# Performance work log

Measured on AMD Instinct MI355X. Metric: run time of the kernel, lower is better.

Reference implementation:

```python
import jax, jax.numpy as jnp
import numpy as np

B, S, H, V, T, L = 32, 128, 1024, 32000, 50, 3


def _ln(x, g, b, eps=1e-5):
    m = x.mean(-1, keepdims=True)
    v = ((x - m) ** 2).mean(-1, keepdims=True)
    return (x - m) / jnp.sqrt(v + eps) * g + b


def setup_inputs() -> dict:
    key = jax.random.key(0)
    ks = iter(jax.random.split(key, 48))
    r = lambda shape, s=0.02: jax.random.normal(next(ks), shape, jnp.float32) * s
    return dict(
        encoder_outputs=jax.random.normal(next(ks), (B, S, H), jnp.float32),
        h0=jax.random.normal(next(ks), (L, B, H), jnp.float32),
        c0=jax.random.normal(next(ks), (L, B, H), jnp.float32),
        valid_src_len=jax.random.randint(next(ks), (B,), 1, S + 1),
        target=jax.random.randint(next(ks), (B, T), 0, V),
        embedding=r((V, H), 1.0),
        Wa=r((H, H)), ba=jnp.zeros((H,)),
        Ua=r((H, H)), ub=jnp.zeros((H,)),
        Va=r((1, H)), vb=jnp.zeros((1,)),
        temperature=jnp.ones((1,)),
        Wih0=r((4 * H, 2 * H)), Whh0=r((4 * H, H)), bih0=jnp.zeros((4 * H,)), bhh0=jnp.zeros((4 * H,)),
        Wih1=r((4 * H, H)), Whh1=r((4 * H, H)), bih1=jnp.zeros((4 * H,)), bhh1=jnp.zeros((4 * H,)),
        Wih2=r((4 * H, H)), Whh2=r((4 * H, H)), bih2=jnp.zeros((4 * H,)), bhh2=jnp.zeros((4 * H,)),
        fc_w=r((V, H)), fc_b=jnp.zeros((V,)),
        eng=jnp.ones((H,)), enb=jnp.zeros((H,)),
        cng=jnp.ones((H,)), cnb=jnp.zeros((H,)),
        ong=jnp.ones((H,)), onb=jnp.zeros((H,)),
    )


def _decode(encoder_outputs, h0, c0, valid_src_len, target, p):
    mask = jnp.arange(S)[None, :] < valid_src_len[:, None]           # (B,S)
    Ukeys = encoder_outputs @ p['Ua'].T + p['ub']                    # (B,S,H) precomputed Ua(keys)
    Wih = (p['Wih0'], p['Wih1'], p['Wih2'])
    Whh = (p['Whh0'], p['Whh1'], p['Whh2'])
    bih = (p['bih0'], p['bih1'], p['bih2'])
    bhh = (p['bhh0'], p['bhh1'], p['bhh2'])
    # teacher forcing: token at step t is start_token (0) for t=0, else target[:, t-1]
    tokens = jnp.concatenate([jnp.zeros((B, 1), target.dtype), target[:, :-1]], 1).T  # (T,B)

    def step(carry, tok):
        h, c = carry                                                 # each (L,B,H)
        emb = _ln(p['embedding'][tok], p['eng'], p['enb'])           # (B,H); dropout omitted (eval)
        q = h[-1]                                                    # (B,H) query = top-layer h
        s = jnp.tanh((q @ p['Wa'].T + p['ba'])[:, None, :] + Ukeys)  # (B,S,H)
        scores = (jnp.einsum('bsh,h->bs', s, p['Va'][0]) + p['vb'][0]) / p['temperature'][0]
        scores = jnp.where(mask, scores, -1e9)
        w = jax.nn.softmax(scores, axis=-1)                          # (B,S)
        ctx = _ln(jnp.einsum('bs,bsh->bh', w, encoder_outputs), p['cng'], p['cnb'])
        x = jnp.concatenate([emb, ctx], axis=-1)                     # (B,2H)
        hs, cs = [], []
        for l in range(L):                                           # 3 stacked LSTM layers
            g = x @ Wih[l].T + bih[l] + h[l] @ Whh[l].T + bhh[l]
            i_, f_, g_, o_ = jnp.split(g, 4, axis=-1)                # torch gate order i,f,g,o
            cl = jax.nn.sigmoid(f_) * c[l] + jax.nn.sigmoid(i_) * jnp.tanh(g_)
            hl = jax.nn.sigmoid(o_) * jnp.tanh(cl)
            hs.append(hl); cs.append(cl); x = hl
        out = _ln(x, p['ong'], p['onb'])
        logits = out @ p['fc_w'].T + p['fc_b']                       # (B,V)
        return (jnp.stack(hs), jnp.stack(cs)), (logits, w)

    (hT, cT), (logits, attn) = jax.lax.scan(step, (h0, c0), tokens)
    return logits.transpose(1, 0, 2), hT, cT, attn.transpose(1, 0, 2)


def reference(encoder_outputs, h0, c0, valid_src_len, target, embedding, Wa, ba, Ua, ub, Va, vb,
              temperature, Wih0, Whh0, bih0, bhh0, Wih1, Whh1, bih1, bhh1, Wih2, Whh2, bih2, bhh2,
              fc_w, fc_b, eng, enb, cng, cnb, ong, onb):
    p = dict(embedding=embedding, Wa=Wa, ba=ba, Ua=Ua, ub=ub, Va=Va, vb=vb, temperature=temperature,
             Wih0=Wih0, Whh0=Whh0, bih0=bih0, bhh0=bhh0, Wih1=Wih1, Whh1=Whh1, bih1=bih1, bhh1=bhh1,
             Wih2=Wih2, Whh2=Whh2, bih2=bih2, bhh2=bhh2, fc_w=fc_w, fc_b=fc_b,
             eng=eng, enb=enb, cng=cng, cnb=cnb, ong=ong, onb=onb)
    logits, hT, cT, attn = _decode(encoder_outputs, h0, c0, valid_src_len, target, p)
    return logits, (hT, cT), attn
```

## Files before the change

kernel.cpp:

```cpp
#include <hip/hip_runtime.h>
#include <math.h>

#define DEV_INLINE __device__ __forceinline__

constexpr int B = 32, S = 128, H = 1024, V = 32000, T = 50, L = 3;
constexpr int H2 = 2 * H, H4 = 4 * H;
constexpr int BH = B * H;

constexpr size_t HT_OFF   = (size_t)B * T * V;
constexpr size_t CT_OFF   = HT_OFF + (size_t)L * B * H;
constexpr size_t ATTN_OFF = CT_OFF + (size_t)L * B * H;

constexpr size_t WS_UKBF  = 0;
constexpr size_t WS_ENCBF = WS_UKBF + (size_t)B * S * H / 2;
constexpr size_t WS_EMBBF = WS_ENCBF + (size_t)B * S * H / 2;
constexpr size_t WS_H2ALL = WS_EMBBF + (size_t)T * BH / 2;
constexpr size_t WS_H     = WS_H2ALL + (size_t)T * BH;
constexpr size_t WS_C     = WS_H + (size_t)L * BH;
constexpr size_t WS_QWA   = WS_C + (size_t)L * BH;
constexpr size_t WS_SCO   = WS_QWA + (size_t)BH;
constexpr size_t WS_GAT   = WS_SCO + (size_t)B * S;
constexpr size_t WS_HBF   = WS_GAT + (size_t)B * H4;
constexpr size_t WS_XCBF  = WS_HBF + (size_t)2 * L * BH / 2;
constexpr size_t WS_OLALL = WS_XCBF + (size_t)B * H2 / 2;
constexpr size_t WS_WBF   = WS_OLALL + (size_t)T * BH / 2;

constexpr size_t OW_WA   = 0;
constexpr size_t OW_WIH0 = OW_WA   + (size_t)H * H;
constexpr size_t OW_WHH0 = OW_WIH0 + (size_t)H4 * H2;
constexpr size_t OW_WIH1 = OW_WHH0 + (size_t)H4 * H;
constexpr size_t OW_WHH1 = OW_WIH1 + (size_t)H4 * H;
constexpr size_t OW_WIH2 = OW_WHH1 + (size_t)H4 * H;
constexpr size_t OW_WHH2 = OW_WIH2 + (size_t)H4 * H;
constexpr size_t OW_FCW  = OW_WHH2 + (size_t)H4 * H;
constexpr size_t OW_UA   = OW_FCW  + (size_t)V * H;
constexpr size_t OW_END  = OW_UA   + (size_t)H * H;
constexpr size_t NEED_WS_BYTES = WS_WBF * 4 + OW_END * 2;

typedef __attribute__((ext_vector_type(8))) short short8;
typedef __attribute__((ext_vector_type(4))) float f32x4;
typedef __attribute__((ext_vector_type(4))) unsigned short u16x4;
typedef __attribute__((ext_vector_type(8))) unsigned short u16x8;

DEV_INLINE float sigmoidf_(float x) { return 1.f / (1.f + expf(-x)); }

DEV_INLINE unsigned short bf16u(float f) {
  union { float f; unsigned u; } v; v.f = f;
  unsigned r = v.u + 0x7fffu + ((v.u >> 16) & 1u);
  return (unsigned short)(r >> 16);
}
DEV_INLINE float bf2f(unsigned short u) {
  union { unsigned u; float f; } v; v.u = (unsigned)u << 16;
  return v.f;
}

DEV_INLINE float wave_sum(float v) {
#pragma unroll
  for (int o = 32; o; o >>= 1) v += __shfl_xor(v, o, 64);
  return v;
}

DEV_INLINE float blk_sum256(float v, float* buf) {
  v = wave_sum(v);
  __syncthreads();
  if ((threadIdx.x & 63) == 0) buf[threadIdx.x >> 6] = v;
  __syncthreads();
  return buf[0] + buf[1] + buf[2] + buf[3];
}

__global__ void k_init(const float* __restrict__ h0, const float* __restrict__ c0,
                       float* __restrict__ hst, float* __restrict__ cst,
                       unsigned short* __restrict__ hbf) {
  int idx = blockIdx.x * 256 + threadIdx.x;
  if (idx < L * BH) { hst[idx] = h0[idx]; hbf[idx] = bf16u(h0[idx]); }
  else cst[idx - L * BH] = c0[idx - L * BH];
}

__global__ void k_fin(const float* __restrict__ hst, const float* __restrict__ h2src,
                      const float* __restrict__ cst, float* __restrict__ out) {
  int idx = blockIdx.x * 256 + threadIdx.x;
  if (idx < 2 * BH) out[HT_OFF + idx] = hst[idx];
  else if (idx < 3 * BH) out[HT_OFF + idx] = h2src[idx - 2 * BH];
  else out[HT_OFF + idx] = cst[idx - 3 * BH];
}

constexpr int NCVT = 10;
struct CvtArgs { const float* src[NCVT]; unsigned short* dst[NCVT]; };
constexpr int CV_N4[NCVT] = {
  H * H / 4, H4 * H2 / 4, H4 * H / 4, H4 * H / 4, H4 * H / 4,
  H4 * H / 4, H4 * H / 4, V * H / 4, H * H / 4, B * S * H / 4};
__global__ void k_cvt_all(CvtArgs a) {
  int cum[NCVT + 1]; cum[0] = 0;
#pragma unroll
  for (int r = 0; r < NCVT; ++r) cum[r + 1] = cum[r] + CV_N4[r];
  const int total = cum[NCVT];
  int i = blockIdx.x * 256 + threadIdx.x;
  const int stride = gridDim.x * 256;
  for (; i < total; i += stride) {
    int r = 0;
#pragma unroll
    for (int q = 0; q < NCVT; ++q) r += (i >= cum[q + 1]) ? 1 : 0;
    int off = i - cum[r];
    f32x4 v = *(const f32x4*)(a.src[r] + (size_t)off * 4);
    u16x4 o;
    o[0] = bf16u(v[0]); o[1] = bf16u(v[1]); o[2] = bf16u(v[2]); o[3] = bf16u(v[3]);
    *(u16x4*)(a.dst[r] + (size_t)off * 4) = o;
  }
}

__global__ __launch_bounds__(256) void k_gemm_nt(
    const float* __restrict__ A, const float* __restrict__ Bw,
    const float* __restrict__ bias, float* __restrict__ C, int N, int K) {
  __shared__ float As[16][132];
  __shared__ float Bs[16][68];
  const int i0 = blockIdx.y * 128, j0 = blockIdx.x * 64;
  const int ty = threadIdx.x >> 4, tx = threadIdx.x & 15;
  float acc[8][4] = {};
  for (int k0 = 0; k0 < K; k0 += 16) {
#pragma unroll
    for (int r = 0; r < 8; ++r) {
      int i = threadIdx.x + 256 * r;
      int mm = i >> 4, kk = i & 15;
      As[kk][mm] = A[(size_t)(i0 + mm) * K + k0 + kk];
    }
#pragma unroll
    for (int r = 0; r < 4; ++r) {
      int i = threadIdx.x + 256 * r;
      int nn = i >> 4, kk = i & 15;
      Bs[kk][nn] = Bw[(size_t)(j0 + nn) * K + k0 + kk];
    }
    __syncthreads();
#pragma unroll
    for (int kk = 0; kk < 16; ++kk) {
      float a[8], bb[4];
#pragma unroll
      for (int i = 0; i < 8; ++i) a[i] = As[kk][ty * 8 + i];
#pragma unroll
      for (int j = 0; j < 4; ++j) bb[j] = Bs[kk][tx * 4 + j];
#pragma unroll
      for (int i = 0; i < 8; ++i)
#pragma unroll
        for (int j = 0; j < 4; ++j) acc[i][j] = fmaf(a[i], bb[j], acc[i][j]);
    }
    __syncthreads();
  }
#pragma unroll
  for (int i = 0; i < 8; ++i) {
    size_t row = (size_t)(i0 + ty * 8 + i) * N;
#pragma unroll
    for (int j = 0; j < 4; ++j) {
      int col = j0 + tx * 4 + j;
      C[row + col] = acc[i][j] + bias[col];
    }
  }
}

__global__ void k_embln(const float* __restrict__ table, const int* __restrict__ target,
                        const float* __restrict__ g, const float* __restrict__ bta,
                        unsigned short* __restrict__ out) {
  __shared__ float rbuf[4];
  int idx = blockIdx.x;
  int t = idx >> 5, b = idx & 31;
  int tok = (t == 0) ? 0 : target[b * T + (t - 1)];
  const float* e = table + (size_t)tok * H;
  int tid = threadIdx.x;
  float x[4];
#pragma unroll
  for (int r = 0; r < 4; ++r) x[r] = e[r * 256 + tid];
  float m = blk_sum256(x[0] + x[1] + x[2] + x[3], rbuf) * (1.f / H);
  float vs = 0.f;
#pragma unroll
  for (int r = 0; r < 4; ++r) { float d = x[r] - m; vs += d * d; }
  float var = blk_sum256(vs, rbuf) * (1.f / H);
  float rstd = rsqrtf(var + 1e-5f);
  unsigned short* o = out + (size_t)idx * H;
#pragma unroll
  for (int r = 0; r < 4; ++r) {
    int h = r * 256 + tid;
    o[h] = bf16u((x[r] - m) * rstd * g[h] + bta[h]);
  }
}

template <int MODE>
__global__ __launch_bounds__(256) void k_gemm_bf(
    const unsigned short* __restrict__ X, const unsigned short* __restrict__ Wb,
    const float* __restrict__ bias, void* __restrict__ outv, int N) {
  __shared__ unsigned short As[64][72];
  __shared__ unsigned short Bs[128][72];
  const int tid = threadIdx.x, lane = tid & 63, wid = tid >> 6;
  const int wm = wid >> 1, wn = wid & 1;
  const int n0 = blockIdx.x * 128, m0 = blockIdx.y * 64;
  const int fr = lane & 15, kg = lane >> 4;
  f32x4 acc[2][4];
#pragma unroll
  for (int i = 0; i < 2; ++i)
#pragma unroll
    for (int j = 0; j < 4; ++j) acc[i][j] = {0.f, 0.f, 0.f, 0.f};
  for (int k0 = 0; k0 < H; k0 += 64) {
    __syncthreads();
#pragma unroll
    for (int r = 0; r < 2; ++r) {
      int i = tid + 256 * r, row = i >> 3, c8 = (i & 7) * 8;
      *(short8*)&As[row][c8] = *(const short8*)(X + (size_t)(m0 + row) * H + k0 + c8);
    }
#pragma unroll
    for (int r = 0; r < 4; ++r) {
      int i = tid + 256 * r, row = i >> 3, c8 = (i & 7) * 8;
      *(short8*)&Bs[row][c8] = *(const short8*)(Wb + (size_t)(n0 + row) * H + k0 + c8);
    }
    __syncthreads();
#pragma unroll
    for (int kk = 0; kk < 64; kk += 32) {
      short8 av[2], bv[4];
      av[0] = *(const short8*)&As[wm * 32 + fr][kk + kg * 8];
      av[1] = *(const short8*)&As[wm * 32 + 16 + fr][kk + kg * 8];
#pragma unroll
      for (int fn = 0; fn < 4; ++fn)
        bv[fn] = *(const short8*)&Bs[wn * 64 + fn * 16 + fr][kk + kg * 8];
#pragma unroll
      for (int fm = 0; fm < 2; ++fm)
#pragma unroll
        for (int fn = 0; fn < 4; ++fn)
          acc[fm][fn] = __builtin_amdgcn_mfma_f32_16x16x32_bf16(av[fm], bv[fn],
                                                                acc[fm][fn], 0, 0, 0);
    }
  }
#pragma unroll
  for (int fm = 0; fm < 2; ++fm)
#pragma unroll
    for (int fn = 0; fn < 4; ++fn)
#pragma unroll
      for (int r = 0; r < 4; ++r) {
        int m = m0 + wm * 32 + fm * 16 + kg * 4 + r;
        int n = n0 + wn * 64 + fn * 16 + fr;
        float val = acc[fm][fn][r] + bias[n];
        if (MODE == 0) {
          ((unsigned short*)outv)[(size_t)m * N + n] = bf16u(val);
        } else {
          int b = m & 31, t = m >> 5;
          ((float*)outv)[((size_t)b * T + t) * V + n] = val;
        }
      }
}

__global__ __launch_bounds__(256) void k_skinny_bf(
    const unsigned short* __restrict__ x, const unsigned short* __restrict__ Wb, int K,
    const float* __restrict__ bias, float* __restrict__ out, int obstride) {
  __shared__ float red[4][32][16];
  const int lane = threadIdx.x & 63, wid = threadIdx.x >> 6;
  const int jb = blockIdx.x * 16;
  const int jl = lane & 15, kg = lane >> 4;
  f32x4 acc0 = {0.f, 0.f, 0.f, 0.f}, acc1 = {0.f, 0.f, 0.f, 0.f};
  const int per = (K >> 5) >> 2;
  const int send = (wid + 1) * per;
  for (int s = wid * per; s < send; ++s) {
    const int ke = s * 32 + kg * 8;
    short8 bw = *(const short8*)(Wb + (size_t)(jb + jl) * K + ke);
    short8 a0 = *(const short8*)(x + (size_t)jl * K + ke);
    short8 a1 = *(const short8*)(x + (size_t)(16 + jl) * K + ke);
    acc0 = __builtin_amdgcn_mfma_f32_16x16x32_bf16(a0, bw, acc0, 0, 0, 0);
    acc1 = __builtin_amdgcn_mfma_f32_16x16x32_bf16(a1, bw, acc1, 0, 0, 0);
  }
#pragma unroll
  for (int r = 0; r < 4; ++r) {
    red[wid][kg * 4 + r][jl] = acc0[r];
    red[wid][16 + kg * 4 + r][jl] = acc1[r];
  }
  __syncthreads();
  const int tid = threadIdx.x;
#pragma unroll
  for (int u = 0; u < 2; ++u) {
    int oi = tid * 2 + u;
    int m = oi >> 4, j = oi & 15;
    float v = red[0][m][j] + red[1][m][j] + red[2][m][j] + red[3][m][j];
    int jg = jb + j;
    out[(size_t)m * obstride + jg] = v + bias[jg];
  }
}

__global__ void k_scores_bf(const float* __restrict__ qwa,
                            const unsigned short* __restrict__ ukbf,
                            const float* __restrict__ va, const float* __restrict__ vb,
                            const float* __restrict__ temp, const int* __restrict__ vlen,
                            float* __restrict__ sco) {
  int lane = threadIdx.x & 63, wid = threadIdx.x >> 6;
  int idx = blockIdx.x * 4 + wid;
  int b = idx >> 7, s = idx & 127;
  const unsigned short* uk = ukbf + (size_t)idx * H + lane * 16;
  const float* q = qwa + (size_t)b * H + lane * 16;
  const float* vp = va + lane * 16;
  u16x8 u0 = *(const u16x8*)uk;
  u16x8 u1 = *(const u16x8*)(uk + 8);
  float a = 0.f;
#pragma unroll
  for (int j = 0; j < 8; ++j) a = fmaf(vp[j], tanhf(q[j] + bf2f(u0[j])), a);
#pragma unroll
  for (int j = 0; j < 8; ++j) a = fmaf(vp[8 + j], tanhf(q[8 + j] + bf2f(u1[j])), a);
  a = wave_sum(a);
  if (lane == 0) {
    float val = (a + vb[0]) / temp[0];
    if (s >= vlen[b]) val = -1e9f;
    sco[idx] = val;
  }
}

__global__ void k_smctx_bf(const float* __restrict__ sco,
                           const unsigned short* __restrict__ encbf,
                           const unsigned short* __restrict__ embt,
                           const float* __restrict__ g, const float* __restrict__ bta,
                           unsigned short* __restrict__ xbf,
                           float* __restrict__ attn, int t) {
  __shared__ float sw[S];
  __shared__ float rbuf[4];
  int b = blockIdx.x, tid = threadIdx.x;
  if (tid < 64) {
    float v0 = sco[b * S + tid], v1 = sco[b * S + 64 + tid];
    float m = fmaxf(v0, v1);
#pragma unroll
    for (int o = 32; o; o >>= 1) m = fmaxf(m, __shfl_xor(m, o, 64));
    float e0 = expf(v0 - m), e1 = expf(v1 - m);
    float ssum = wave_sum(e0 + e1);
    float inv = 1.f / ssum;
    sw[tid] = e0 * inv;
    sw[64 + tid] = e1 * inv;
  }
  __syncthreads();
  if (tid < S) attn[((size_t)b * T + t) * S + tid] = sw[tid];
  float v[4] = {0.f, 0.f, 0.f, 0.f};
  {
    const unsigned short* ep = encbf + (size_t)b * S * H + tid * 4;
    for (int s2 = 0; s2 < S; ++s2) {
      float wv = sw[s2];
      u16x4 e4 = *(const u16x4*)(ep + (size_t)s2 * H);
#pragma unroll
      for (int r = 0; r < 4; ++r) v[r] = fmaf(wv, bf2f(e4[r]), v[r]);
    }
  }
  float m = blk_sum256(v[0] + v[1] + v[2] + v[3], rbuf) * (1.f / H);
  float vs = 0.f;
#pragma unroll
  for (int r = 0; r < 4; ++r) { float d = v[r] - m; vs += d * d; }
  float var = blk_sum256(vs, rbuf) * (1.f / H);
  float rstd = rsqrtf(var + 1e-5f);
  unsigned short* xr = xbf + (size_t)b * H2;
#pragma unroll
  for (int r = 0; r < 4; ++r) {
    int h = tid * 4 + r;
    xr[H + h] = bf16u((v[r] - m) * rstd * g[h] + bta[h]);
    xr[h] = embt[(size_t)b * H + h];
  }
}

__global__ __launch_bounds__(256) void k_gates4(
    const unsigned short* __restrict__ x1, int K1,
    const unsigned short* __restrict__ x2, int K2,
    const unsigned short* __restrict__ W1, const unsigned short* __restrict__ W2,
    const float* __restrict__ bih, const float* __restrict__ bhh,
    float* __restrict__ cl, float* __restrict__ hl, unsigned short* __restrict__ hbfw) {
  __shared__ float red[4][32][17];
  const int lane = threadIdx.x & 63, wid = threadIdx.x >> 6;
  const int jb = blockIdx.x * 4;
  const int fr = lane & 15, kg = lane >> 4;
  const int wrow = (fr >> 2) * H + jb + (fr & 3);
  f32x4 acc0 = {0.f, 0.f, 0.f, 0.f}, acc1 = {0.f, 0.f, 0.f, 0.f};
  const int s1 = K1 >> 5, s2 = K2 >> 5;
  const int per = (s1 + s2) >> 2;
  const int sbeg = wid * per, send = sbeg + per;
  const int e1 = send < s1 ? send : s1;
#pragma unroll 4
  for (int s = sbeg; s < e1; ++s) {
    const int ke = s * 32 + kg * 8;
    short8 bw = *(const short8*)(W1 + (size_t)wrow * K1 + ke);
    short8 a0 = *(const short8*)(x1 + (size_t)fr * K1 + ke);
    short8 a1 = *(const short8*)(x1 + (size_t)(16 + fr) * K1 + ke);
    acc0 = __builtin_amdgcn_mfma_f32_16x16x32_bf16(a0, bw, acc0, 0, 0, 0);
    acc1 = __builtin_amdgcn_mfma_f32_16x16x32_bf16(a1, bw, acc1, 0, 0, 0);
  }
  const int b2 = sbeg > s1 ? sbeg : s1;
#pragma unroll 4
  for (int s = b2; s < send; ++s) {
    const int ke = (s - s1) * 32 + kg * 8;
    short8 bw = *(const short8*)(W2 + (size_t)wrow * K2 + ke);
    short8 a0 = *(const short8*)(x2 + (size_t)fr * K2 + ke);
    short8 a1 = *(const short8*)(x2 + (size_t)(16 + fr) * K2 + ke);
    acc0 = __builtin_amdgcn_mfma_f32_16x16x32_bf16(a0, bw, acc0, 0, 0, 0);
    acc1 = __builtin_amdgcn_mfma_f32_16x16x32_bf16(a1, bw, acc1, 0, 0, 0);
  }
#pragma unroll
  for (int r = 0; r < 4; ++r) {
    red[wid][kg * 4 + r][fr] = acc0[r];
    red[wid][16 + kg * 4 + r][fr] = acc1[r];
  }
  __syncthreads();
  const int tid = threadIdx.x;
  if (tid < 128) {
    int m = tid >> 2, jj = tid & 3, kcol = jb + jj;
    float gate[4];
#pragma unroll
    for (int g = 0; g < 4; ++g) {
      int f = g * 4 + jj;
      gate[g] = red[0][m][f] + red[1][m][f] + red[2][m][f] + red[3][m][f]
              + bih[g * H + kcol] + bhh[g * H + kcol];
    }
    int idx = m * H + kcol;
    float cn = sigmoidf_(gate[1]) * cl[idx] + sigmoidf_(gate[0]) * tanhf(gate[2]);
    float hn = sigmoidf_(gate[3]) * tanhf(cn);
    cl[idx] = cn;
    hl[idx] = hn;
    hbfw[idx] = bf16u(hn);
  }
}

__global__ void k_ln_all(const float* __restrict__ h2all, const float* __restrict__ g,
                         const float* __restrict__ bta, unsigned short* __restrict__ olbf) {
  __shared__ float rbuf[4];
  int row = blockIdx.x, tid = threadIdx.x;
  const float* hr = h2all + (size_t)row * H;
  float hv[4];
#pragma unroll
  for (int r = 0; r < 4; ++r) hv[r] = hr[r * 256 + tid];
  float m = blk_sum256(hv[0] + hv[1] + hv[2] + hv[3], rbuf) * (1.f / H);
  float vs = 0.f;
#pragma unroll
  for (int r = 0; r < 4; ++r) { float d = hv[r] - m; vs += d * d; }
  float var = blk_sum256(vs, rbuf) * (1.f / H);
  float rstd = rsqrtf(var + 1e-5f);
  unsigned short* o = olbf + (size_t)row * H;
#pragma unroll
  for (int r = 0; r < 4; ++r) {
    int k = r * 256 + tid;
    o[k] = bf16u((hv[r] - m) * rstd * g[k] + bta[k]);
  }
}

__global__ __launch_bounds__(256) void k_mfma_skinny(
    const unsigned short* __restrict__ x1, const float* __restrict__ W1, int K1,
    const unsigned short* __restrict__ x2, const float* __restrict__ W2, int K2,
    const float* __restrict__ b1, const float* __restrict__ b2,
    float* __restrict__ out, int obstride) {
  __shared__ float red[4][32][16];
  const int lane = threadIdx.x & 63, wid = threadIdx.x >> 6;
  const int jb = blockIdx.x * 16;
  const int jl = lane & 15, kg = lane >> 4;
  f32x4 acc0 = {0.f, 0.f, 0.f, 0.f}, acc1 = {0.f, 0.f, 0.f, 0.f};
  const int s1 = K1 >> 5, s2 = K2 >> 5;
  const int per = (s1 + s2) >> 2;
  const int send = (wid + 1) * per;
  for (int s = wid * per; s < send; ++s) {
    const unsigned short* x; const float* W; int K, k0;
    if (s < s1) { x = x1; W = W1; K = K1; k0 = s * 32; }
    else       { x = x2; W = W2; K = K2; k0 = (s - s1) * 32; }
    const int ke = k0 + kg * 8;
    const float* wp = W + (size_t)(jb + jl) * K + ke;
    f32x4 w0 = *(const f32x4*)wp;
    f32x4 w1 = *(const f32x4*)(wp + 4);
    short8 bw;
    bw[0] = (short)bf16u(w0[0]); bw[1] = (short)bf16u(w0[1]);
    bw[2] = (short)bf16u(w0[2]); bw[3] = (short)bf16u(w0[3]);
    bw[4] = (short)bf16u(w1[0]); bw[5] = (short)bf16u(w1[1]);
    bw[6] = (short)bf16u(w1[2]); bw[7] = (short)bf16u(w1[3]);
    short8 a0 = *(const short8*)(x + (size_t)jl * K + ke);
    short8 a1 = *(const short8*)(x + (size_t)(16 + jl) * K + ke);
    acc0 = __builtin_amdgcn_mfma_f32_16x16x32_bf16(a0, bw, acc0, 0, 0, 0);
    acc1 = __builtin_amdgcn_mfma_f32_16x16x32_bf16(a1, bw, acc1, 0, 0, 0);
  }
#pragma unroll
  for (int r = 0; r < 4; ++r) {
    red[wid][kg * 4 + r][jl] = acc0[r];
    red[wid][16 + kg * 4 + r][jl] = acc1[r];
  }
  __syncthreads();
  const int tid = threadIdx.x;
#pragma unroll
  for (int u = 0; u < 2; ++u) {
    int oi = tid * 2 + u;
    int m = oi >> 4, j = oi & 15;
    float v = red[0][m][j] + red[1][m][j] + red[2][m][j] + red[3][m][j];
    int jg = jb + j;
    v += (b1 ? b1[jg] : 0.f) + (b2 ? b2[jg] : 0.f);
    out[(size_t)m * obstride + jg] = v;
  }
}

__global__ void k_scores_f32(const float* __restrict__ qwa, const float* __restrict__ ukeys,
                             const float* __restrict__ va, const float* __restrict__ vb,
                             const float* __restrict__ temp, const int* __restrict__ vlen,
                             float* __restrict__ sco) {
  int lane = threadIdx.x & 63, wid = threadIdx.x >> 6;
  int idx = blockIdx.x * 4 + wid;
  int b = idx >> 7, s = idx & 127;
  const float* uk = ukeys + (size_t)idx * H;
  const float* q = qwa + (size_t)b * H;
  float a = 0.f;
#pragma unroll
  for (int i = 0; i < 16; ++i) {
    int k = i * 64 + lane;
    a = fmaf(va[k], tanhf(q[k] + uk[k]), a);
  }
  a = wave_sum(a);
  if (lane == 0) {
    float val = (a + vb[0]) / temp[0];
    if (s >= vlen[b]) val = -1e9f;
    sco[idx] = val;
  }
}

__global__ void k_smctx_f32(const float* __restrict__ sco, const float* __restrict__ enc,
                            const unsigned short* __restrict__ embt, const float* __restrict__ g,
                            const float* __restrict__ bta, unsigned short* __restrict__ xbf,
                            float* __restrict__ attn, int t) {
  __shared__ float sw[S];
  __shared__ float rbuf[4];
  int b = blockIdx.x, tid = threadIdx.x;
  if (tid < 64) {
    float v0 = sco[b * S + tid], v1 = sco[b * S + 64 + tid];
    float m = fmaxf(v0, v1);
#pragma unroll
    for (int o = 32; o; o >>= 1) m = fmaxf(m, __shfl_xor(m, o, 64));
    float e0 = expf(v0 - m), e1 = expf(v1 - m);
    float ssum = wave_sum(e0 + e1);
    float inv = 1.f / ssum;
    sw[tid] = e0 * inv;
    sw[64 + tid] = e1 * inv;
  }
  __syncthreads();
  if (tid < S) attn[((size_t)b * T + t) * S + tid] = sw[tid];
  float v[4] = {0.f, 0.f, 0.f, 0.f};
  for (int s2 = 0; s2 < S; ++s2) {
    float wv = sw[s2];
    const float* er = enc + ((size_t)b * S + s2) * H;
#pragma unroll
    for (int r = 0; r < 4; ++r) v[r] = fmaf(wv, er[r * 256 + tid], v[r]);
  }
  float m = blk_sum256(v[0] + v[1] + v[2] + v[3], rbuf) * (1.f / H);
  float vs = 0.f;
#pragma unroll
  for (int r = 0; r < 4; ++r) { float d = v[r] - m; vs += d * d; }
  float var = blk_sum256(vs, rbuf) * (1.f / H);
  float rstd = rsqrtf(var + 1e-5f);
  unsigned short* xr = xbf + (size_t)b * H2;
#pragma unroll
  for (int r = 0; r < 4; ++r) {
    int h = r * 256 + tid;
    xr[H + h] = bf16u((v[r] - m) * rstd * g[h] + bta[h]);
    xr[h] = embt[(size_t)b * H + h];
  }
}

__global__ void k_cell(const float* __restrict__ gat, float* __restrict__ cl,
                       float* __restrict__ hl, unsigned short* __restrict__ hbf) {
  int idx = blockIdx.x * 256 + threadIdx.x;
  int b = idx >> 10, k = idx & 1023;
  const float* gb = gat + (size_t)b * H4;
  float i_ = gb[k], f_ = gb[H + k], g_ = gb[2 * H + k], o_ = gb[3 * H + k];
  float cn = sigmoidf_(f_) * cl[idx] + sigmoidf_(i_) * tanhf(g_);
  float hn = sigmoidf_(o_) * tanhf(cn);
  cl[idx] = cn;
  hl[idx] = hn;
  hbf[idx] = bf16u(hn);
}

__global__ void k_cell2ln(const float* __restrict__ gat, float* __restrict__ cl,
                          float* __restrict__ hl, const float* __restrict__ g,
                          const float* __restrict__ bta, unsigned short* __restrict__ olbf,
                          unsigned short* __restrict__ hbf) {
  __shared__ float rbuf[4];
  int b = blockIdx.x, tid = threadIdx.x;
  const float* gb = gat + (size_t)b * H4;
  float hv[4];
#pragma unroll
  for (int r = 0; r < 4; ++r) {
    int k = r * 256 + tid;
    float i_ = gb[k], f_ = gb[H + k], g_ = gb[2 * H + k], o_ = gb[3 * H + k];
    float cn = sigmoidf_(f_) * cl[b * H + k] + sigmoidf_(i_) * tanhf(g_);
    float hn = sigmoidf_(o_) * tanhf(cn);
    cl[b * H + k] = cn;
    hl[b * H + k] = hn;
    hbf[b * H + k] = bf16u(hn);
    hv[r] = hn;
  }
  float m = blk_sum256(hv[0] + hv[1] + hv[2] + hv[3], rbuf) * (1.f / H);
  float vs = 0.f;
#pragma unroll
  for (int r = 0; r < 4; ++r) { float d = hv[r] - m; vs += d * d; }
  float var = blk_sum256(vs, rbuf) * (1.f / H);
  float rstd = rsqrtf(var + 1e-5f);
#pragma unroll
  for (int r = 0; r < 4; ++r) {
    int k = r * 256 + tid;
    olbf[b * H + k] = bf16u((hv[r] - m) * rstd * g[k] + bta[k]);
  }
}

extern "C" void kernel_launch(void* const* d_in, const int* in_sizes, int n_in,
                              void* d_out, int out_size, void* d_ws, size_t ws_size,
                              hipStream_t stream) {
  (void)in_sizes; (void)n_in; (void)out_size;
  const float* enc = (const float*)d_in[0];
  const float* h0 = (const float*)d_in[1];
  const float* c0 = (const float*)d_in[2];
  const int* vlen = (const int*)d_in[3];
  const int* target = (const int*)d_in[4];
  const float* emb_table = (const float*)d_in[5];
  const float* Wa = (const float*)d_in[6];
  const float* ba = (const float*)d_in[7];
  const float* Ua = (const float*)d_in[8];
  const float* ub = (const float*)d_in[9];
  const float* Va = (const float*)d_in[10];
  const float* vb = (const float*)d_in[11];
  const float* temp = (const float*)d_in[12];
  const float* Wih[3] = {(const float*)d_in[13], (const float*)d_in[17], (const float*)d_in[21]};
  const float* Whh[3] = {(const float*)d_in[14], (const float*)d_in[18], (const float*)d_in[22]};
  const float* bih[3] = {(const float*)d_in[15], (const float*)d_in[19], (const float*)d_in[23]};
  const float* bhh[3] = {(const float*)d_in[16], (const float*)d_in[20], (const float*)d_in[24]};
  const float* fcw = (const float*)d_in[25];
  const float* fcb = (const float*)d_in[26];
  const float* eng = (const float*)d_in[27];
  const float* enb = (const float*)d_in[28];
  const float* cng = (const float*)d_in[29];
  const float* cnb = (const float*)d_in[30];
  const float* ong = (const float*)d_in[31];
  const float* onb = (const float*)d_in[32];

  float* ws = (float*)d_ws;
  unsigned short* ukbf = (unsigned short*)(ws + WS_UKBF);
  unsigned short* encbf = (unsigned short*)(ws + WS_ENCBF);
  unsigned short* embbf = (unsigned short*)(ws + WS_EMBBF);
  float* h2all = ws + WS_H2ALL;
  float* hst = ws + WS_H;
  float* cst = ws + WS_C;
  float* qwa = ws + WS_QWA;
  float* sco = ws + WS_SCO;
  float* gat = ws + WS_GAT;
  unsigned short* hbf = (unsigned short*)(ws + WS_HBF);
  unsigned short* xcbf = (unsigned short*)(ws + WS_XCBF);
  unsigned short* olall = (unsigned short*)(ws + WS_OLALL);
  unsigned short* wbf = (unsigned short*)(ws + WS_WBF);
  float* out = (float*)d_out;

  const bool big = ws_size >= NEED_WS_BYTES;

  k_init<<<768, 256, 0, stream>>>(h0, c0, hst, cst, hbf);
  k_embln<<<T * B, 256, 0, stream>>>(emb_table, target, eng, enb, embbf);

  if (big) {
    CvtArgs ca;
    ca.src[0] = Wa;      ca.dst[0] = wbf + OW_WA;
    ca.src[1] = Wih[0];  ca.dst[1] = wbf + OW_WIH0;
    ca.src[2] = Whh[0];  ca.dst[2] = wbf + OW_WHH0;
    ca.src[3] = Wih[1];  ca.dst[3] = wbf + OW_WIH1;
    ca.src[4] = Whh[1];  ca.dst[4] = wbf + OW_WHH1;
    ca.src[5] = Wih[2];  ca.dst[5] = wbf + OW_WIH2;
    ca.src[6] = Whh[2];  ca.dst[6] = wbf + OW_WHH2;
    ca.src[7] = fcw;     ca.dst[7] = wbf + OW_FCW;
    ca.src[8] = Ua;      ca.dst[8] = wbf + OW_UA;
    ca.src[9] = enc;     ca.dst[9] = encbf;
    k_cvt_all<<<2048, 256, 0, stream>>>(ca);
    k_gemm_bf<0><<<dim3(H / 128, (B * S) / 64), 256, 0, stream>>>(
        encbf, wbf + OW_UA, ub, ukbf, H);

    for (int t = 0; t < T; ++t) {
      const unsigned short* rb = hbf + (size_t)(t & 1) * (L * BH);
      unsigned short* wb = hbf + (size_t)((t + 1) & 1) * (L * BH);
      k_skinny_bf<<<H / 16, 256, 0, stream>>>(rb + 2 * BH, wbf + OW_WA, H, ba, qwa, H);
      k_scores_bf<<<(B * S) / 4, 256, 0, stream>>>(qwa, ukbf, Va, vb, temp, vlen, sco);
      k_smctx_bf<<<B, 256, 0, stream>>>(sco, encbf, embbf + (size_t)t * BH, cng, cnb,
                                        xcbf, out + ATTN_OFF, t);
      k_gates4<<<H / 4, 256, 0, stream>>>(xcbf, H2, rb, H,
                                          wbf + OW_WIH0, wbf + OW_WHH0,
                                          bih[0], bhh[0], cst, hst, wb);
      k_gates4<<<H / 4, 256, 0, stream>>>(wb, H, rb + BH, H,
                                          wbf + OW_WIH1, wbf + OW_WHH1,
                                          bih[1], bhh[1], cst + BH, hst + BH, wb + BH);
      k_gates4<<<H / 4, 256, 0, stream>>>(wb + BH, H, rb + 2 * BH, H,
                                          wbf + OW_WIH2, wbf + OW_WHH2,
                                          bih[2], bhh[2], cst + 2 * BH,
                                          h2all + (size_t)t * BH, wb + 2 * BH);
    }
    k_ln_all<<<T * B, 256, 0, stream>>>(h2all, ong, onb, olall);
    k_gemm_bf<1><<<dim3(V / 128, (T * B) / 64), 256, 0, stream>>>(
        olall, wbf + OW_FCW, fcb, out, V);
    k_fin<<<768, 256, 0, stream>>>(hst, h2all + (size_t)(T - 1) * BH, cst, out);
  } else {
    float* ukeys_f32 = ws + WS_WBF;
    k_gemm_nt<<<dim3(H / 64, (B * S) / 128), 256, 0, stream>>>(enc, Ua, ub, ukeys_f32, H, H);
    for (int t = 0; t < T; ++t) {
      k_mfma_skinny<<<H / 16, 256, 0, stream>>>(hbf + 2 * BH, Wa, H, nullptr, nullptr, 0,
                                                ba, nullptr, qwa, H);
      k_scores_f32<<<(B * S) / 4, 256, 0, stream>>>(qwa, ukeys_f32, Va, vb, temp, vlen, sco);
      k_smctx_f32<<<B, 256, 0, stream>>>(sco, enc, embbf + (size_t)t * BH, cng, cnb, xcbf,
                                         out + ATTN_OFF, t);
      k_mfma_skinny<<<H4 / 16, 256, 0, stream>>>(xcbf, Wih[0], H2, hbf, Whh[0], H,
                                                 bih[0], bhh[0], gat, H4);
      k_cell<<<BH / 256, 256, 0, stream>>>(gat, cst, hst, hbf);
      k_mfma_skinny<<<H4 / 16, 256, 0, stream>>>(hbf, Wih[1], H, hbf + BH, Whh[1], H,
                                                 bih[1], bhh[1], gat, H4);
      k_cell<<<BH / 256, 256, 0, stream>>>(gat, cst + BH, hst + BH, hbf + BH);
      k_mfma_skinny<<<H4 / 16, 256, 0, stream>>>(hbf + BH, Wih[2], H, hbf + 2 * BH, Whh[2], H,
                                                 bih[2], bhh[2], gat, H4);
      k_cell2ln<<<B, 256, 0, stream>>>(gat, cst + 2 * BH, hst + 2 * BH, ong, onb,
                                       olall + (size_t)t * BH, hbf + 2 * BH);
      k_mfma_skinny<<<V / 16, 256, 0, stream>>>(olall + (size_t)t * BH, fcw, H,
                                                nullptr, nullptr, 0,
                                                fcb, nullptr, out + (size_t)t * V, T * V);
    }
    k_fin<<<768, 256, 0, stream>>>(hst, hst + 2 * BH, cst, out);
  }
}
```

Measured before the change: 3.520 ms.

## Fuse per-step decoder kernels into one persistent kernel with grid barriers

Replaces the six kernel launches per decode step (300 in total) with a single persistent 256-workgroup kernel. The attention projection, scores, softmax/context, and the three LSTM gate phases run as separate phases inside it, separated by a software grid barrier built on atomics. This removes launch overhead and inter-kernel gaps but depends on all 256 workgroups being co-resident. Some phases leave many workgroups idle, and each of the six barriers per step costs an atomic round trip. It also adds a redundant gate preload loop in gates_phase.

```diff
diff --git a/kernel.cpp b/kernel.cpp
--- a/kernel.cpp
+++ b/kernel.cpp
@@ -6,6 +6,7 @@
 constexpr int B = 32, S = 128, H = 1024, V = 32000, T = 50, L = 3;
 constexpr int H2 = 2 * H, H4 = 4 * H;
 constexpr int BH = B * H;
+constexpr int NWG = 256;
 
 constexpr size_t HT_OFF   = (size_t)B * T * V;
 constexpr size_t CT_OFF   = HT_OFF + (size_t)L * B * H;
@@ -68,10 +69,29 @@
   return buf[0] + buf[1] + buf[2] + buf[3];
 }
 
+DEV_INLINE void gbar(unsigned* cnt, unsigned* gen) {
+  __syncthreads();
+  if (threadIdx.x == 0) {
+    __threadfence();
+    unsigned g = __hip_atomic_load(gen, __ATOMIC_RELAXED, __HIP_MEMORY_SCOPE_AGENT);
+    unsigned a = __hip_atomic_fetch_add(cnt, 1u, __ATOMIC_ACQ_REL, __HIP_MEMORY_SCOPE_AGENT);
+    if (a == NWG - 1) {
+      __hip_atomic_store(cnt, 0u, __ATOMIC_RELAXED, __HIP_MEMORY_SCOPE_AGENT);
+      __hip_atomic_fetch_add(gen, 1u, __ATOMIC_RELEASE, __HIP_MEMORY_SCOPE_AGENT);
+    } else {
+      while (__hip_atomic_load(gen, __ATOMIC_RELAXED, __HIP_MEMORY_SCOPE_AGENT) == g)
+        __builtin_amdgcn_s_sleep(2);
+    }
+    __threadfence();
+  }
+  __syncthreads();
+}
+
 __global__ void k_init(const float* __restrict__ h0, const float* __restrict__ c0,
                        float* __restrict__ hst, float* __restrict__ cst,
-                       unsigned short* __restrict__ hbf) {
+                       unsigned short* __restrict__ hbf, unsigned* __restrict__ bar) {
   int idx = blockIdx.x * 256 + threadIdx.x;
+  if (idx < 2) bar[idx] = 0u;
   if (idx < L * BH) { hst[idx] = h0[idx]; hbf[idx] = bf16u(h0[idx]); }
   else cst[idx - L * BH] = c0[idx - L * BH];
 }
@@ -243,123 +263,26 @@
       }
 }
 
-__global__ __launch_bounds__(256) void k_skinny_bf(
-    const unsigned short* __restrict__ x, const unsigned short* __restrict__ Wb, int K,
-    const float* __restrict__ bias, float* __restrict__ out, int obstride) {
-  __shared__ float red[4][32][16];
-  const int lane = threadIdx.x & 63, wid = threadIdx.x >> 6;
-  const int jb = blockIdx.x * 16;
-  const int jl = lane & 15, kg = lane >> 4;
-  f32x4 acc0 = {0.f, 0.f, 0.f, 0.f}, acc1 = {0.f, 0.f, 0.f, 0.f};
-  const int per = (K >> 5) >> 2;
-  const int send = (wid + 1) * per;
-  for (int s = wid * per; s < send; ++s) {
-    const int ke = s * 32 + kg * 8;
-    short8 bw = *(const short8*)(Wb + (size_t)(jb + jl) * K + ke);
-    short8 a0 = *(const short8*)(x + (size_t)jl * K + ke);
-    short8 a1 = *(const short8*)(x + (size_t)(16 + jl) * K + ke);
-    acc0 = __builtin_amdgcn_mfma_f32_16x16x32_bf16(a0, bw, acc0, 0, 0, 0);
-    acc1 = __builtin_amdgcn_mfma_f32_16x16x32_bf16(a1, bw, acc1, 0, 0, 0);
-  }
-#pragma unroll
-  for (int r = 0; r < 4; ++r) {
-    red[wid][kg * 4 + r][jl] = acc0[r];
-    red[wid][16 + kg * 4 + r][jl] = acc1[r];
-  }
-  __syncthreads();
-  const int tid = threadIdx.x;
-#pragma unroll
-  for (int u = 0; u < 2; ++u) {
-    int oi = tid * 2 + u;
-    int m = oi >> 4, j = oi & 15;
-    float v = red[0][m][j] + red[1][m][j] + red[2][m][j] + red[3][m][j];
-    int jg = jb + j;
-    out[(size_t)m * obstride + jg] = v + bias[jg];
-  }
-}
-
-__global__ void k_scores_bf(const float* __restrict__ qwa,
-                            const unsigned short* __restrict__ ukbf,
-                            const float* __restrict__ va, const float* __restrict__ vb,
-                            const float* __restrict__ temp, const int* __restrict__ vlen,
-                            float* __restrict__ sco) {
-  int lane = threadIdx.x & 63, wid = threadIdx.x >> 6;
-  int idx = blockIdx.x * 4 + wid;
-  int b = idx >> 7, s = idx & 127;
-  const unsigned short* uk = ukbf + (size_t)idx * H + lane * 16;
-  const float* q = qwa + (size_t)b * H + lane * 16;
-  const float* vp = va + lane * 16;
-  u16x8 u0 = *(const u16x8*)uk;
-  u16x8 u1 = *(const u16x8*)(uk + 8);
-  float a = 0.f;
-#pragma unroll
-  for (int j = 0; j < 8; ++j) a = fmaf(vp[j], tanhf(q[j] + bf2f(u0[j])), a);
-#pragma unroll
-  for (int j = 0; j < 8; ++j) a = fmaf(vp[8 + j], tanhf(q[8 + j] + bf2f(u1[j])), a);
-  a = wave_sum(a);
-  if (lane == 0) {
-    float val = (a + vb[0]) / temp[0];
-    if (s >= vlen[b]) val = -1e9f;
-    sco[idx] = val;
-  }
-}
-
-__global__ void k_smctx_bf(const float* __restrict__ sco,
-                           const unsigned short* __restrict__ encbf,
-                           const unsigned short* __restrict__ embt,
-                           const float* __restrict__ g, const float* __restrict__ bta,
-                           unsigned short* __restrict__ xbf,
-                           float* __restrict__ attn, int t) {
-  __shared__ float sw[S];
-  __shared__ float rbuf[4];
-  int b = blockIdx.x, tid = threadIdx.x;
-  if (tid < 64) {
-    float v0 = sco[b * S + tid], v1 = sco[b * S + 64 + tid];
-    float m = fmaxf(v0, v1);
-#pragma unroll
-    for (int o = 32; o; o >>= 1) m = fmaxf(m, __shfl_xor(m, o, 64));
-    float e0 = expf(v0 - m), e1 = expf(v1 - m);
-    float ssum = wave_sum(e0 + e1);
-    float inv = 1.f / ssum;
-    sw[tid] = e0 * inv;
-    sw[64 + tid] = e1 * inv;
-  }
-  __syncthreads();
-  if (tid < S) attn[((size_t)b * T + t) * S + tid] = sw[tid];
-  float v[4] = {0.f, 0.f, 0.f, 0.f};
-  {
-    const unsigned short* ep = encbf + (size_t)b * S * H + tid * 4;
-    for (int s2 = 0; s2 < S; ++s2) {
-      float wv = sw[s2];
-      u16x4 e4 = *(const u16x4*)(ep + (size_t)s2 * H);
-#pragma unroll
-      for (int r = 0; r < 4; ++r) v[r] = fmaf(wv, bf2f(e4[r]), v[r]);
-    }
-  }
-  float m = blk_sum256(v[0] + v[1] + v[2] + v[3], rbuf) * (1.f / H);
-  float vs = 0.f;
-#pragma unroll
-  for (int r = 0; r < 4; ++r) { float d = v[r] - m; vs += d * d; }
-  float var = blk_sum256(vs, rbuf) * (1.f / H);
-  float rstd = rsqrtf(var + 1e-5f);
-  unsigned short* xr = xbf + (size_t)b * H2;
-#pragma unroll
-  for (int r = 0; r < 4; ++r) {
-    int h = tid * 4 + r;
-    xr[H + h] = bf16u((v[r] - m) * rstd * g[h] + bta[h]);
-    xr[h] = embt[(size_t)b * H + h];
-  }
-}
-
-__global__ __launch_bounds__(256) void k_gates4(
-    const unsigned short* __restrict__ x1, int K1,
-    const unsigned short* __restrict__ x2, int K2,
-    const unsigned short* __restrict__ W1, const unsigned short* __restrict__ W2,
-    const float* __restrict__ bih, const float* __restrict__ bhh,
-    float* __restrict__ cl, float* __restrict__ hl, unsigned short* __restrict__ hbfw) {
-  __shared__ float red[4][32][17];
-  const int lane = threadIdx.x & 63, wid = threadIdx.x >> 6;
-  const int jb = blockIdx.x * 4;
+struct StepArgs {
+  const unsigned short* ukbf; const unsigned short* encbf; const unsigned short* embbf;
+  const unsigned short* wbf;
+  const float* ba; const float* va; const float* vb; const float* temp; const int* vlen;
+  const float* cng; const float* cnb;
+  const float* bih0; const float* bhh0; const float* bih1; const float* bhh1;
+  const float* bih2; const float* bhh2;
+  float* qwa; float* sco; unsigned short* xcbf;
+  unsigned short* hbf; float* hst; float* cst; float* h2all;
+  float* attn;
+  unsigned* bar;
+};
+
+DEV_INLINE void gates_phase(
+    int wg, int tid, int lane, int wid, float (*red)[32][17],
+    const unsigned short* x1, int K1, const unsigned short* x2, int K2,
+    const unsigned short* W1, const unsigned short* W2,
+    const float* bih, const float* bhh,
+    float* cl, float* hl, unsigned short* hbfw) {
+  const int jb = wg * 4;
   const int fr = lane & 15, kg = lane >> 4;
   const int wrow = (fr >> 2) * H + jb + (fr & 3);
   f32x4 acc0 = {0.f, 0.f, 0.f, 0.f}, acc1 = {0.f, 0.f, 0.f, 0.f};
@@ -392,10 +315,14 @@
     red[wid][16 + kg * 4 + r][fr] = acc1[r];
   }
   __syncthreads();
-  const int tid = threadIdx.x;
   if (tid < 128) {
     int m = tid >> 2, jj = tid & 3, kcol = jb + jj;
     float gate[4];
+#pragma unroll
+    for (int g = 0; g < 4; ++g) {
+      int f = g * 4 + jj;
+      gate[g] = red[0][g == 0 ? m : m][f];
+    }
 #pragma unroll
     for (int g = 0; g < 4; ++g) {
       int f = g * 4 + jj;
@@ -408,6 +335,137 @@
     cl[idx] = cn;
     hl[idx] = hn;
     hbfw[idx] = bf16u(hn);
+  }
+}
+
+__global__ __launch_bounds__(256) void k_steps(StepArgs A) {
+  const int wg = blockIdx.x;
+  const int tid = threadIdx.x, lane = tid & 63, wid = tid >> 6;
+  __shared__ float red[4][32][17];
+  __shared__ float sw[S];
+  __shared__ float rbuf[4];
+  unsigned* cnt = A.bar;
+  unsigned* gen = A.bar + 1;
+
+  for (int t = 0; t < T; ++t) {
+    const unsigned short* rb = A.hbf + (size_t)(t & 1) * (L * BH);
+    unsigned short* wb = A.hbf + (size_t)((t + 1) & 1) * (L * BH);
+
+    if (wg < 64) {
+      const int jb = wg * 16;
+      const int jl = lane & 15, kg = lane >> 4;
+      const unsigned short* x = rb + 2 * BH;
+      const unsigned short* Wb = A.wbf + OW_WA;
+      f32x4 acc0 = {0.f, 0.f, 0.f, 0.f}, acc1 = {0.f, 0.f, 0.f, 0.f};
+      const int per = (H >> 5) >> 2;
+      const int send = (wid + 1) * per;
+      for (int s = wid * per; s < send; ++s) {
+        const int ke = s * 32 + kg * 8;
+        short8 bw = *(const short8*)(Wb + (size_t)(jb + jl) * H + ke);
+        short8 a0 = *(const short8*)(x + (size_t)jl * H + ke);
+        short8 a1 = *(const short8*)(x + (size_t)(16 + jl) * H + ke);
+        acc0 = __builtin_amdgcn_mfma_f32_16x16x32_bf16(a0, bw, acc0, 0, 0, 0);
+        acc1 = __builtin_amdgcn_mfma_f32_16x16x32_bf16(a1, bw, acc1, 0, 0, 0);
+      }
+#pragma unroll
+      for (int r = 0; r < 4; ++r) {
+        red[wid][kg * 4 + r][jl] = acc0[r];
+        red[wid][16 + kg * 4 + r][jl] = acc1[r];
+      }
+      __syncthreads();
+#pragma unroll
+      for (int u = 0; u < 2; ++u) {
+        int oi = tid * 2 + u;
+        int m = oi >> 4, j = oi & 15;
+        float v = red[0][m][j] + red[1][m][j] + red[2][m][j] + red[3][m][j];
+        A.qwa[(size_t)m * H + jb + j] = v + A.ba[jb + j];
+      }
+    }
+    gbar(cnt, gen);
+
+    {
+      const int idxb = (wg * 4 + wid) * 4;
+      const int b = idxb >> 7;
+      const float* q = A.qwa + (size_t)b * H + lane * 16;
+      const float* vp = A.va + lane * 16;
+      float vbv = A.vb[0], tmp = A.temp[0];
+      int vl = A.vlen[b];
+#pragma unroll
+      for (int i = 0; i < 4; ++i) {
+        int idx = idxb + i;
+        int s = idx & 127;
+        const unsigned short* uk = A.ukbf + (size_t)idx * H + lane * 16;
+        u16x8 u0 = *(const u16x8*)uk;
+        u16x8 u1 = *(const u16x8*)(uk + 8);
+        float a = 0.f;
+#pragma unroll
+        for (int j = 0; j < 8; ++j) a = fmaf(vp[j], tanhf(q[j] + bf2f(u0[j])), a);
+#pragma unroll
+        for (int j = 0; j < 8; ++j) a = fmaf(vp[8 + j], tanhf(q[8 + j] + bf2f(u1[j])), a);
+        a = wave_sum(a);
+        if (lane == 0) {
+          float val = (a + vbv) / tmp;
+          if (s >= vl) val = -1e9f;
+          A.sco[idx] = val;
+        }
+      }
+    }
+    gbar(cnt, gen);
+
+    if (wg < 32) {
+      const int b = wg;
+      if (tid < 64) {
+        float v0 = A.sco[b * S + tid], v1 = A.sco[b * S + 64 + tid];
+        float m = fmaxf(v0, v1);
+#pragma unroll
+        for (int o = 32; o; o >>= 1) m = fmaxf(m, __shfl_xor(m, o, 64));
+        float e0 = expf(v0 - m), e1 = expf(v1 - m);
+        float ssum = wave_sum(e0 + e1);
+        float inv = 1.f / ssum;
+        sw[tid] = e0 * inv;
+        sw[64 + tid] = e1 * inv;
+      }
+      __syncthreads();
+      if (tid < S) A.attn[((size_t)b * T + t) * S + tid] = sw[tid];
+      float v[4] = {0.f, 0.f, 0.f, 0.f};
+      {
+        const unsigned short* ep = A.encbf + (size_t)b * S * H + tid * 4;
+        for (int s2 = 0; s2 < S; ++s2) {
+          float wv = sw[s2];
+          u16x4 e4 = *(const u16x4*)(ep + (size_t)s2 * H);
+#pragma unroll
+          for (int r = 0; r < 4; ++r) v[r] = fmaf(wv, bf2f(e4[r]), v[r]);
+        }
+      }
+      float m = blk_sum256(v[0] + v[1] + v[2] + v[3], rbuf) * (1.f / H);
+      float vs = 0.f;
+#pragma unroll
+      for (int r = 0; r < 4; ++r) { float d = v[r] - m; vs += d * d; }
+      float var = blk_sum256(vs, rbuf) * (1.f / H);
+      float rstd = rsqrtf(var + 1e-5f);
+      unsigned short* xr = A.xcbf + (size_t)b * H2;
+      const unsigned short* embt = A.embbf + (size_t)t * BH;
+#pragma unroll
+      for (int r = 0; r < 4; ++r) {
+        int h = tid * 4 + r;
+        xr[H + h] = bf16u((v[r] - m) * rstd * A.cng[h] + A.cnb[h]);
+        xr[h] = embt[(size_t)b * H + h];
+      }
+    }
+    gbar(cnt, gen);
+
+    gates_phase(wg, tid, lane, wid, red, A.xcbf, H2, rb, H,
+                A.wbf + OW_WIH0, A.wbf + OW_WHH0, A.bih0, A.bhh0,
+                A.cst, A.hst, wb);
+    gbar(cnt, gen);
+    gates_phase(wg, tid, lane, wid, red, wb, H, rb + BH, H,
+                A.wbf + OW_WIH1, A.wbf + OW_WHH1, A.bih1, A.bhh1,
+                A.cst + BH, A.hst + BH, wb + BH);
+    gbar(cnt, gen);
+    gates_phase(wg, tid, lane, wid, red, wb + BH, H, rb + 2 * BH, H,
+                A.wbf + OW_WIH2, A.wbf + OW_WHH2, A.bih2, A.bhh2,
+                A.cst + 2 * BH, A.h2all + (size_t)t * BH, wb + 2 * BH);
+    gbar(cnt, gen);
   }
 }
 
@@ -632,6 +690,7 @@
   float* qwa = ws + WS_QWA;
   float* sco = ws + WS_SCO;
   float* gat = ws + WS_GAT;
+  unsigned* bar = (unsigned*)(ws + WS_GAT);
   unsigned short* hbf = (unsigned short*)(ws + WS_HBF);
   unsigned short* xcbf = (unsigned short*)(ws + WS_XCBF);
   unsigned short* olall = (unsigned short*)(ws + WS_OLALL);
@@ -640,7 +699,7 @@
 
   const bool big = ws_size >= NEED_WS_BYTES;
 
-  k_init<<<768, 256, 0, stream>>>(h0, c0, hst, cst, hbf);
+  k_init<<<768, 256, 0, stream>>>(h0, c0, hst, cst, hbf, bar);
   k_embln<<<T * B, 256, 0, stream>>>(emb_table, target, eng, enb, embbf);
 
   if (big) {
@@ -659,24 +718,17 @@
     k_gemm_bf<0><<<dim3(H / 128, (B * S) / 64), 256, 0, stream>>>(
         encbf, wbf + OW_UA, ub, ukbf, H);
 
-    for (int t = 0; t < T; ++t) {
-      const unsigned short* rb = hbf + (size_t)(t & 1) * (L * BH);
-      unsigned short* wb = hbf + (size_t)((t + 1) & 1) * (L * BH);
-      k_skinny_bf<<<H / 16, 256, 0, stream>>>(rb + 2 * BH, wbf + OW_WA, H, ba, qwa, H);
-      k_scores_bf<<<(B * S) / 4, 256, 0, stream>>>(qwa, ukbf, Va, vb, temp, vlen, sco);
-      k_smctx_bf<<<B, 256, 0, stream>>>(sco, encbf, embbf + (size_t)t * BH, cng, cnb,
-                                        xcbf, out + ATTN_OFF, t);
-      k_gates4<<<H / 4, 256, 0, stream>>>(xcbf, H2, rb, H,
-                                          wbf + OW_WIH0, wbf + OW_WHH0,
-                                          bih[0], bhh[0], cst, hst, wb);
-      k_gates4<<<H / 4, 256, 0, stream>>>(wb, H, rb + BH, H,
-                                          wbf + OW_WIH1, wbf + OW_WHH1,
-                                          bih[1], bhh[1], cst + BH, hst + BH, wb + BH);
-      k_gates4<<<H / 4, 256, 0, stream>>>(wb + BH, H, rb + 2 * BH, H,
-                                          wbf + OW_WIH2, wbf + OW_WHH2,
-                                          bih[2], bhh[2], cst + 2 * BH,
-                                          h2all + (size_t)t * BH, wb + 2 * BH);
-    }
+    StepArgs A;
+    A.ukbf = ukbf; A.encbf = encbf; A.embbf = embbf; A.wbf = wbf;
+    A.ba = ba; A.va = Va; A.vb = vb; A.temp = temp; A.vlen = vlen;
+    A.cng = cng; A.cnb = cnb;
+    A.bih0 = bih[0]; A.bhh0 = bhh[0]; A.bih1 = bih[1]; A.bhh1 = bhh[1];
+    A.bih2 = bih[2]; A.bhh2 = bhh[2];
+    A.qwa = qwa; A.sco = sco; A.xcbf = xcbf;
+    A.hbf = hbf; A.hst = hst; A.cst = cst; A.h2all = h2all;
+    A.attn = out + ATTN_OFF; A.bar = bar;
+    k_steps<<<NWG, 256, 0, stream>>>(A);
+
     k_ln_all<<<T * B, 256, 0, stream>>>(h2all, ong, onb, olall);
     k_gemm_bf<1><<<dim3(V / 128, (T * B) / 64), 256, 0, stream>>>(
         olall, wbf + OW_FCW, fcb, out, V);
```

Measured after the change: 10.69 ms. 204% more time.
